# Kernel optimization log

Measured on AMD Instinct MI355X. Metric: run time of the kernel, lower is better.

## Reference

```python
import jax, jax.numpy as jnp
import numpy as np

N = 50000          # nodes
E_RAND = 800000    # random edges (avg degree 16)
D_IN = 128
H = 4              # heads (both layers)
C = 64             # per-head channels (both layers)
NEG_SLOPE = 0.2    # PyG GATConv default leaky_relu slope


def _gat_conv(x, src, dst, W, att_src, att_dst, bias, concat):
    """PyG GATConv (dropout=0, self-loops already in edge list).
    x:[N,Din] W:[Din,H*C] att_*:[H,C] bias:[H*C] or [C]."""
    n = x.shape[0]
    h = (x @ W).reshape(n, H, C)                      # [N,H,C]
    a_src = jnp.sum(h * att_src, axis=-1)             # [N,H]
    a_dst = jnp.sum(h * att_dst, axis=-1)             # [N,H]
    e = jax.nn.leaky_relu(a_src[src] + a_dst[dst], NEG_SLOPE)  # [E,H]
    # segment softmax over incoming edges of each destination node
    m = jax.ops.segment_max(e, dst, num_segments=n)    # [N,H]
    e = jnp.exp(e - m[dst])
    denom = jax.ops.segment_sum(e, dst, num_segments=n)
    alpha = e / (denom[dst] + 1e-16)                   # [E,H]
    msg = h[src] * alpha[..., None]                    # [E,H,C]
    out = jax.ops.segment_sum(msg, dst, num_segments=n)  # [N,H,C]
    if concat:
        out = out.reshape(n, H * C)
    else:
        out = out.mean(axis=1)
    return out + bias


def setup_inputs() -> dict:
    key = jax.random.key(0)
    ks = jax.random.split(key, 10)
    x = jax.random.normal(ks[0], (N, D_IN), jnp.float32)
    src = jax.random.randint(ks[1], (E_RAND,), 0, N)
    dst = jax.random.randint(ks[2], (E_RAND,), 0, N)
    loops = jnp.arange(N)  # add_self_loops=True (PyG default)
    edge_index = jnp.stack([jnp.concatenate([src, loops]),
                            jnp.concatenate([dst, loops])]).astype(jnp.int32)
    g = lambda k, shp, fan: (jax.random.normal(k, shp, jnp.float32) / np.float32(np.sqrt(fan)))
    W1 = g(ks[3], (D_IN, H * C), D_IN)
    att_src1 = g(ks[4], (H, C), C)
    att_dst1 = g(ks[5], (H, C), C)
    b1 = jnp.zeros((H * C,), jnp.float32)
    W2 = g(ks[6], (H * C, H * C), H * C)
    att_src2 = g(ks[7], (H, C), C)
    att_dst2 = g(ks[8], (H, C), C)
    b2 = jnp.zeros((C,), jnp.float32)
    return {"x": x, "edge_index": edge_index,
            "W1": W1, "att_src1": att_src1, "att_dst1": att_dst1, "b1": b1,
            "W2": W2, "att_src2": att_src2, "att_dst2": att_dst2, "b2": b2}


def reference(x, edge_index, W1, att_src1, att_dst1, b1, W2, att_src2, att_dst2, b2):
    src, dst = edge_index[0], edge_index[1]
    h = jax.nn.relu(_gat_conv(x, src, dst, W1, att_src1, att_dst1, b1, concat=True))
    h = jax.nn.relu(_gat_conv(h, src, dst, W2, att_src2, att_dst2, b2, concat=False))
    return jax.nn.softmax(h, axis=1)
```

## Files before the change

### kernel.cpp

```cpp
#include <hip/hip_runtime.h>


typedef __attribute__((ext_vector_type(8))) short short8;
typedef __attribute__((ext_vector_type(4))) float f32x4;
typedef __attribute__((ext_vector_type(2))) float f32x2;

static __device__ __forceinline__ ushort f2bf(float f) {
  uint u = __float_as_uint(f);
  return (ushort)((u + 0x7FFFu + ((u >> 16) & 1u)) >> 16);
}
static __device__ __forceinline__ float bf2f(ushort s) {
  return __uint_as_float(((uint)s) << 16);
}
static __device__ __forceinline__ unsigned char f2fp8(float f) {
  int p = __builtin_amdgcn_cvt_pk_fp8_f32(f, f, 0, false);
  return (unsigned char)(p & 0xFF);
}
static __device__ __forceinline__ uint4 cvt8bf(const float4& a, const float4& b) {
  uint4 hh;
  hh.x = (uint)f2bf(a.x) | ((uint)f2bf(a.y) << 16);
  hh.y = (uint)f2bf(a.z) | ((uint)f2bf(a.w) << 16);
  hh.z = (uint)f2bf(b.x) | ((uint)f2bf(b.y) << 16);
  hh.w = (uint)f2bf(b.z) | ((uint)f2bf(b.w) << 16);
  return hh;
}
static __device__ __forceinline__ void gl16(const ushort* g, ushort* l) {
  __builtin_amdgcn_global_load_lds(
      (const __attribute__((address_space(1))) uint*)(g),
      (__attribute__((address_space(3))) uint*)(l), 16, 0, 0);
}

__global__ __launch_bounds__(256)
void k_prep(const float* __restrict__ W1, const float* __restrict__ W2,
            ushort* __restrict__ w1t, ushort* __restrict__ w2t,
            const float* __restrict__ x, ushort* __restrict__ xb,
            int* __restrict__ cnt, int N,
            int ng , int xcb) {
  const int b = blockIdx.x;
  if (b < 128) {
    int gid = b * 256 + threadIdx.x;
    int c = gid & 255, k = gid >> 8;
    w1t[(size_t)c * 128 + k] = f2bf(W1[(size_t)k * 256 + c]);
  } else if (b < 384) {
    int gid = (b - 128) * 256 + threadIdx.x;
    int c = gid & 255, k = gid >> 8;
    w2t[(size_t)c * 256 + k] = f2bf(W2[(size_t)k * 256 + c]);
  } else if (b < 384 + xcb) {
    int i = (b - 384) * 256 + threadIdx.x;
    if (i < ng) {
      const float4* xp = (const float4*)x + (size_t)i * 2;
      float4 a = xp[0], bb = xp[1];
      ((uint4*)xb)[i] = cvt8bf(a, bb);
    }
  } else {
    int i = (b - 384 - xcb) * 1024 + threadIdx.x;
#pragma unroll
    for (int k = 0; k < 4; k++) {
      int j = i + k * 256;
      if (j < N) cnt[j] = 0;
    }
  }
}

template <int K>
static __device__ __forceinline__
void gemm_body(int bid, const ushort* __restrict__ Ah,
               const ushort* __restrict__ Bt,
               unsigned char* __restrict__ hout, int Nrows,
               const float* __restrict__ att_s, const float* __restrict__ att_d,
               float* __restrict__ a_s, float* __restrict__ a_d) {
  __shared__ ushort Asb[2][128][32];
  __shared__ ushort Bhb[2][128][32];

  const int nrb = (Nrows + 127) >> 7;
  const int rb = (bid >> 4) * 8 + (bid & 7);
  const int ch = (bid >> 3) & 1;
  if (rb >= nrb) return;
  const int row0 = rb * 128;
  const int col0 = ch * 128;

  const int t = threadIdx.x;
  const int lane = t & 63;
  const int w = t >> 6;
  const int wr = (w >> 1) * 64;
  const int wc = (w & 1) * 64;
  const int fr = lane & 15;
  const int fq = lane >> 4;

  const int srow = lane >> 2;
  const int skc = (lane & 3) * 8;
  int ar0 = row0 + w * 32 + srow;
  int ar1 = ar0 + 16;
  ar0 = ar0 < Nrows ? ar0 : Nrows - 1;
  ar1 = ar1 < Nrows ? ar1 : Nrows - 1;
  const ushort* agp0 = Ah + (size_t)ar0 * K + skc;
  const ushort* agp1 = Ah + (size_t)ar1 * K + skc;
  const ushort* bhg0 = Bt + (size_t)(col0 + w * 32 + srow) * K + skc;
  const ushort* bhg1 = bhg0 + (size_t)16 * K;

  f32x4 acc[4][4] = {};

  auto stage = [&](int buf, int k0) {
    gl16(agp0 + k0, &Asb[buf][w * 32][0]);
    gl16(agp1 + k0, &Asb[buf][w * 32 + 16][0]);
    gl16(bhg0 + k0, &Bhb[buf][w * 32][0]);
    gl16(bhg1 + k0, &Bhb[buf][w * 32 + 16][0]);
  };

  stage(0, 0);
  const int NK = K / 32;
#pragma unroll
  for (int ks = 0; ks < NK; ks++) {
    const int buf = ks & 1;
    __syncthreads();
    if (ks + 1 < NK) stage(buf ^ 1, (ks + 1) * 32);

    short8 fa[4], fbh[4];
#pragma unroll
    for (int r = 0; r < 4; r++)
      fa[r] = *(const short8*)(&Asb[buf][wr + r * 16 + fr][fq * 8]);
#pragma unroll
    for (int c = 0; c < 4; c++)
      fbh[c] = *(const short8*)(&Bhb[buf][wc + c * 16 + fr][fq * 8]);
#pragma unroll
    for (int r = 0; r < 4; r++)
#pragma unroll
      for (int c = 0; c < 4; c++)
        acc[r][c] = __builtin_amdgcn_mfma_f32_16x16x32_bf16(fa[r], fbh[c], acc[r][c], 0, 0, 0);
  }

#pragma unroll
  for (int r = 0; r < 4; r++)
#pragma unroll
    for (int c = 0; c < 4; c++) {
      int colg = col0 + wc + c * 16 + fr;
#pragma unroll
      for (int reg = 0; reg < 4; reg++) {
        int gr = row0 + wr + r * 16 + fq * 4 + reg;
        if (gr < Nrows)
          hout[(size_t)gr * 256 + colg] = f2fp8(acc[r][c][reg]);
      }
    }

  const int head = (col0 + wc) >> 6;
  float asv[4], adv[4];
#pragma unroll
  for (int c = 0; c < 4; c++) {
    asv[c] = att_s[col0 + wc + c * 16 + fr];
    adv[c] = att_d[col0 + wc + c * 16 + fr];
  }
#pragma unroll
  for (int r = 0; r < 4; r++)
#pragma unroll
    for (int reg = 0; reg < 4; reg++) {
      float ps = 0.f, pd = 0.f;
#pragma unroll
      for (int c = 0; c < 4; c++) {
        ps += acc[r][c][reg] * asv[c];
        pd += acc[r][c][reg] * adv[c];
      }
      ps += __shfl_xor(ps, 1); pd += __shfl_xor(pd, 1);
      ps += __shfl_xor(ps, 2); pd += __shfl_xor(pd, 2);
      ps += __shfl_xor(ps, 4); pd += __shfl_xor(pd, 4);
      ps += __shfl_xor(ps, 8); pd += __shfl_xor(pd, 8);
      if (fr == 0) {
        int gr = row0 + wr + r * 16 + fq * 4 + reg;
        if (gr < Nrows) {
          a_s[(size_t)gr * 4 + head] = ps;
          a_d[(size_t)gr * 4 + head] = pd;
        }
      }
    }
}

__global__ __launch_bounds__(256)
void k_gemm1_hist(const ushort* __restrict__ xb,
                  const ushort* __restrict__ Bt,
                  unsigned char* __restrict__ hout, int Nrows,
                  const float* __restrict__ att_s,
                  const float* __restrict__ att_d,
                  float* __restrict__ a_s, float* __restrict__ a_d,
                  const int* __restrict__ srcv, const int* __restrict__ dstv,
                  int* __restrict__ cnt, int* __restrict__ col2,
                  int E, int gemm_blocks) {
  if ((int)blockIdx.x < gemm_blocks) {
    gemm_body<128>(blockIdx.x, xb, Bt, hout, Nrows,
                   att_s, att_d, a_s, a_d);
  } else {
    int base = ((int)blockIdx.x - gemm_blocks) * 2048 + threadIdx.x;
    int d[8], v[8], s[8];
#pragma unroll
    for (int k = 0; k < 8; k++) {
      int i = base + k * 256;
      bool ok = i < E;
      d[k] = ok ? dstv[i] : 0;
      v[k] = ok ? (srcv[i] << 8) : 0;
    }
#pragma unroll
    for (int k = 0; k < 8; k++) {
      int i = base + k * 256;
      s[k] = (i < E) ? atomicAdd(&cnt[d[k]], 1) : 64;
    }
#pragma unroll
    for (int k = 0; k < 8; k++) {
      int i = base + k * 256;
      if (i < E && s[k] < 64) col2[(d[k] << 6) + s[k]] = v[k];
    }
  }
}

__global__ __launch_bounds__(256)
void k_gemm2(const ushort* __restrict__ Ah,
             const ushort* __restrict__ Bt,
             unsigned char* __restrict__ hout, int Nrows,
             const float* __restrict__ att_s, const float* __restrict__ att_d,
             float* __restrict__ a_s, float* __restrict__ a_d) {
  gemm_body<256>(blockIdx.x, Ah, Bt, hout, Nrows,
                 att_s, att_d, a_s, a_d);
}

template <int LAYER>
__global__ __launch_bounds__(256)
void k_aggr(const unsigned char* __restrict__ hsrc,
            const int* __restrict__ cnt, const int* __restrict__ col2,
            const float* __restrict__ a_s, const float* __restrict__ a_d,
            const float* __restrict__ bias,
            ushort* __restrict__ out_h, float* __restrict__ outp, int N) {
  __shared__ int   s_sh[4][64];
  __shared__ float w_sh[4][256];
  const int wv = threadIdx.x >> 6;
  const int lane = threadIdx.x & 63;
  const int node = blockIdx.x * 4 + wv;
  if (node >= N) return;
  const int hd = lane >> 4;
  const int deg = min(cnt[node], 64);
  const int beg = node << 6;
  const float4 adst = *(const float4*)(a_d + (size_t)node * 4);

  f32x2 accA = {0.f, 0.f};
  f32x2 accB = {0.f, 0.f};
  float wsum = 0.f;
  const char* hbase = (const char*)hsrc + lane * 4;

  {
    int nc = deg;
    int off = 0;
    float4 w4 = make_float4(0.f, 0.f, 0.f, 0.f);
    if (lane < nc) {
      off = col2[beg + lane];
      const float4 a = *(const float4*)((const char*)a_s + (size_t)((uint)off >> 4));
      float e0 = a.x + adst.x; e0 = e0 > 0.f ? e0 : 0.2f * e0;
      float e1 = a.y + adst.y; e1 = e1 > 0.f ? e1 : 0.2f * e1;
      float e2 = a.z + adst.z; e2 = e2 > 0.f ? e2 : 0.2f * e2;
      float e3 = a.w + adst.w; e3 = e3 > 0.f ? e3 : 0.2f * e3;
      w4 = make_float4(__expf(e0), __expf(e1), __expf(e2), __expf(e3));
    }
    s_sh[wv][lane] = off;
    *(float4*)(&w_sh[wv][lane * 4]) = w4;
    asm volatile("s_waitcnt lgkmcnt(0)" ::: "memory");

    const float* wrow = &w_sh[wv][hd];
    const int*   srow = &s_sh[wv][0];
    int j = 0;
    for (; j + 8 <= nc; j += 8) {
      int o0 = srow[j],     o1 = srow[j + 1], o2 = srow[j + 2], o3 = srow[j + 3];
      int o4 = srow[j + 4], o5 = srow[j + 5], o6 = srow[j + 6], o7 = srow[j + 7];
      float ww0 = wrow[4 * j],      ww1 = wrow[4 * j + 4];
      float ww2 = wrow[4 * j + 8],  ww3 = wrow[4 * j + 12];
      float ww4 = wrow[4 * j + 16], ww5 = wrow[4 * j + 20];
      float ww6 = wrow[4 * j + 24], ww7 = wrow[4 * j + 28];
      uint p0 = *(const uint*)(hbase + (size_t)(uint)o0);
      uint p1 = *(const uint*)(hbase + (size_t)(uint)o1);
      uint p2 = *(const uint*)(hbase + (size_t)(uint)o2);
      uint p3 = *(const uint*)(hbase + (size_t)(uint)o3);
      uint p4 = *(const uint*)(hbase + (size_t)(uint)o4);
      uint p5 = *(const uint*)(hbase + (size_t)(uint)o5);
      uint p6 = *(const uint*)(hbase + (size_t)(uint)o6);
      uint p7 = *(const uint*)(hbase + (size_t)(uint)o7);
      wsum += ww0 + ww1 + ww2 + ww3;
      wsum += ww4 + ww5 + ww6 + ww7;
      f32x2 W;
#define EDGE_FMA(ww, p)                                                     \
      {                                                                     \
        f32x2 lo = __builtin_amdgcn_cvt_pk_f32_fp8((p), false);             \
        f32x2 hi = __builtin_amdgcn_cvt_pk_f32_fp8((p), true);              \
        W.x = (ww); W.y = (ww);                                             \
        accA = __builtin_elementwise_fma(W, lo, accA);                      \
        accB = __builtin_elementwise_fma(W, hi, accB);                      \
      }
      EDGE_FMA(ww0, p0) EDGE_FMA(ww1, p1) EDGE_FMA(ww2, p2) EDGE_FMA(ww3, p3)
      EDGE_FMA(ww4, p4) EDGE_FMA(ww5, p5) EDGE_FMA(ww6, p6) EDGE_FMA(ww7, p7)
    }
    for (; j + 4 <= nc; j += 4) {
      int o0 = srow[j], o1 = srow[j + 1], o2 = srow[j + 2], o3 = srow[j + 3];
      float ww0 = wrow[4 * j],     ww1 = wrow[4 * j + 4];
      float ww2 = wrow[4 * j + 8], ww3 = wrow[4 * j + 12];
      uint p0 = *(const uint*)(hbase + (size_t)(uint)o0);
      uint p1 = *(const uint*)(hbase + (size_t)(uint)o1);
      uint p2 = *(const uint*)(hbase + (size_t)(uint)o2);
      uint p3 = *(const uint*)(hbase + (size_t)(uint)o3);
      wsum += ww0 + ww1 + ww2 + ww3;
      f32x2 W;
      EDGE_FMA(ww0, p0) EDGE_FMA(ww1, p1) EDGE_FMA(ww2, p2) EDGE_FMA(ww3, p3)
    }
    for (; j < nc; j++) {
      int o = srow[j];
      float ww = wrow[4 * j];
      uint p = *(const uint*)(hbase + (size_t)(uint)o);
      wsum += ww;
      f32x2 W;
      EDGE_FMA(ww, p)
    }
#undef EDGE_FMA
  }

  float inv = 1.0f / wsum;
  float4 v = make_float4(accA.x * inv, accA.y * inv, accB.x * inv, accB.y * inv);

  if (LAYER == 1) {
    const float4 bv = *(const float4*)(bias + lane * 4);
    v.x = fmaxf(v.x + bv.x, 0.f);
    v.y = fmaxf(v.y + bv.y, 0.f);
    v.z = fmaxf(v.z + bv.z, 0.f);
    v.w = fmaxf(v.w + bv.w, 0.f);
    ushort4 h;
    h.x = f2bf(v.x); h.y = f2bf(v.y); h.z = f2bf(v.z); h.w = f2bf(v.w);
    *(ushort4*)(out_h + (size_t)node * 256 + lane * 4) = h;
  } else {
    v.x += __shfl_xor(v.x, 16); v.y += __shfl_xor(v.y, 16);
    v.z += __shfl_xor(v.z, 16); v.w += __shfl_xor(v.w, 16);
    v.x += __shfl_xor(v.x, 32); v.y += __shfl_xor(v.y, 32);
    v.z += __shfl_xor(v.z, 32); v.w += __shfl_xor(v.w, 32);
    const int c4 = (lane & 15) * 4;
    const float4 bv = *(const float4*)(bias + c4);
    v.x = fmaxf(v.x * 0.25f + bv.x, 0.f);
    v.y = fmaxf(v.y * 0.25f + bv.y, 0.f);
    v.z = fmaxf(v.z * 0.25f + bv.z, 0.f);
    v.w = fmaxf(v.w * 0.25f + bv.w, 0.f);
    float mx = fmaxf(fmaxf(v.x, v.y), fmaxf(v.z, v.w));
    for (int off = 8; off >= 1; off >>= 1) mx = fmaxf(mx, __shfl_xor(mx, off));
    v.x = __expf(v.x - mx); v.y = __expf(v.y - mx);
    v.z = __expf(v.z - mx); v.w = __expf(v.w - mx);
    float sum = v.x + v.y + v.z + v.w;
    for (int off = 8; off >= 1; off >>= 1) sum += __shfl_xor(sum, off);
    float is = 1.0f / sum;
    v.x *= is; v.y *= is; v.z *= is; v.w *= is;
    if (lane < 16) *(float4*)(outp + (size_t)node * 64 + c4) = v;
  }
}


extern "C" void kernel_launch(void* const* d_in, const int* in_sizes, int n_in,
                              void* d_out, int out_size, void* d_ws, size_t ws_size,
                              hipStream_t stream) {
  const float* x   = (const float*)d_in[0];
  const int*   ei  = (const int*)d_in[1];
  const float* W1  = (const float*)d_in[2];
  const float* as1 = (const float*)d_in[3];
  const float* ad1 = (const float*)d_in[4];
  const float* b1  = (const float*)d_in[5];
  const float* W2  = (const float*)d_in[6];
  const float* as2 = (const float*)d_in[7];
  const float* ad2 = (const float*)d_in[8];
  const float* b2  = (const float*)d_in[9];
  float* out = (float*)d_out;

  const int N = in_sizes[0] / 128;
  const int E = in_sizes[1] / 2;
  const int* srcv = ei;
  const int* dstv = ei + E;

  unsigned char* h8 = (unsigned char*)d_ws;
  ushort* hb   = (ushort*)(h8 + (size_t)N * 256);
  ushort* w1t  = hb + (size_t)N * 256;
  ushort* w2t  = w1t + 256 * 128;
  float*  zbuf = (float*)(w2t + 256 * 256);
  float* a_s1 = zbuf;
  float* a_d1 = a_s1 + (size_t)N * 4;
  float* a_s2 = a_d1 + (size_t)N * 4;
  float* a_d2 = a_s2 + (size_t)N * 4;
  int* cnt    = (int*)(zbuf + (size_t)N * 16);
  int* col2   = cnt + N;
  ushort* xb  = (ushort*)(col2 + (size_t)N * 64);

  const int eb8 = (E + 2047) / 2048;
  const int ng = N * 16;
  const int xcb = (ng + 255) / 256;
  const int zb  = (N + 1023) / 1024;

  const int nrb = (N + 127) / 128;
  const int gemm_blocks = ((nrb + 7) / 8) * 16;
  const int wb = (N + 3) / 4;

  k_prep<<<384 + xcb + zb, 256, 0, stream>>>(W1, W2, w1t, w2t,
                                             x, xb, cnt, N, ng, xcb);
  k_gemm1_hist<<<gemm_blocks + eb8, 256, 0, stream>>>(
      xb, w1t, h8, N, as1, ad1, a_s1, a_d1,
      srcv, dstv, cnt, col2, E, gemm_blocks);
  k_aggr<1><<<wb, 256, 0, stream>>>(h8, cnt, col2, a_s1, a_d1, b1,
                                    hb, nullptr, N);
  k_gemm2<<<gemm_blocks, 256, 0, stream>>>(hb, w2t, h8, N,
                                           as2, ad2, a_s2, a_d2);
  k_aggr<2><<<wb, 256, 0, stream>>>(h8, cnt, col2, a_s2, a_d2, b2,
                                    nullptr, out, N);
}
```

Baseline: 249.7 us.

## Move edge histogram into prep kernel and zero counts with memset

```diff
diff --git a/kernel.cpp b/kernel.cpp
--- a/kernel.cpp
+++ b/kernel.cpp
@@ -31,33 +31,47 @@
 }
 
 __global__ __launch_bounds__(256)
-void k_prep(const float* __restrict__ W1, const float* __restrict__ W2,
-            ushort* __restrict__ w1t, ushort* __restrict__ w2t,
-            const float* __restrict__ x, ushort* __restrict__ xb,
-            int* __restrict__ cnt, int N,
-            int ng , int xcb) {
+void k_prep_hist(const float* __restrict__ W1, const float* __restrict__ W2,
+                 ushort* __restrict__ w1t, ushort* __restrict__ w2t,
+                 const float* __restrict__ x, ushort* __restrict__ xb,
+                 const int* __restrict__ srcv, const int* __restrict__ dstv,
+                 int* __restrict__ cnt, int* __restrict__ col2,
+                 int E, int ng, int eb8) {
   const int b = blockIdx.x;
-  if (b < 128) {
-    int gid = b * 256 + threadIdx.x;
+  if (b < eb8) {
+    int base = b * 2048 + threadIdx.x;
+    int d[8], v[8], s[8];
+#pragma unroll
+    for (int k = 0; k < 8; k++) {
+      int i = base + k * 256;
+      bool ok = i < E;
+      d[k] = ok ? dstv[i] : 0;
+      v[k] = ok ? (srcv[i] << 8) : 0;
+    }
+#pragma unroll
+    for (int k = 0; k < 8; k++) {
+      int i = base + k * 256;
+      s[k] = (i < E) ? atomicAdd(&cnt[d[k]], 1) : 64;
+    }
+#pragma unroll
+    for (int k = 0; k < 8; k++) {
+      int i = base + k * 256;
+      if (i < E && s[k] < 64) col2[(d[k] << 6) + s[k]] = v[k];
+    }
+  } else if (b < eb8 + 128) {
+    int gid = (b - eb8) * 256 + threadIdx.x;
     int c = gid & 255, k = gid >> 8;
     w1t[(size_t)c * 128 + k] = f2bf(W1[(size_t)k * 256 + c]);
-  } else if (b < 384) {
-    int gid = (b - 128) * 256 + threadIdx.x;
+  } else if (b < eb8 + 384) {
+    int gid = (b - eb8 - 128) * 256 + threadIdx.x;
     int c = gid & 255, k = gid >> 8;
     w2t[(size_t)c * 256 + k] = f2bf(W2[(size_t)k * 256 + c]);
-  } else if (b < 384 + xcb) {
-    int i = (b - 384) * 256 + threadIdx.x;
+  } else {
+    int i = (b - eb8 - 384) * 256 + threadIdx.x;
     if (i < ng) {
       const float4* xp = (const float4*)x + (size_t)i * 2;
       float4 a = xp[0], bb = xp[1];
       ((uint4*)xb)[i] = cvt8bf(a, bb);
-    }
-  } else {
-    int i = (b - 384 - xcb) * 1024 + threadIdx.x;
-#pragma unroll
-    for (int k = 0; k < 4; k++) {
-      int j = i + k * 256;
-      if (j < N) cnt[j] = 0;
     }
   }
 }
@@ -174,49 +188,19 @@
 }
 
 __global__ __launch_bounds__(256)
-void k_gemm1_hist(const ushort* __restrict__ xb,
-                  const ushort* __restrict__ Bt,
-                  unsigned char* __restrict__ hout, int Nrows,
-                  const float* __restrict__ att_s,
-                  const float* __restrict__ att_d,
-                  float* __restrict__ a_s, float* __restrict__ a_d,
-                  const int* __restrict__ srcv, const int* __restrict__ dstv,
-                  int* __restrict__ cnt, int* __restrict__ col2,
-                  int E, int gemm_blocks) {
-  if ((int)blockIdx.x < gemm_blocks) {
-    gemm_body<128>(blockIdx.x, xb, Bt, hout, Nrows,
-                   att_s, att_d, a_s, a_d);
-  } else {
-    int base = ((int)blockIdx.x - gemm_blocks) * 2048 + threadIdx.x;
-    int d[8], v[8], s[8];
-#pragma unroll
-    for (int k = 0; k < 8; k++) {
-      int i = base + k * 256;
-      bool ok = i < E;
-      d[k] = ok ? dstv[i] : 0;
-      v[k] = ok ? (srcv[i] << 8) : 0;
-    }
-#pragma unroll
-    for (int k = 0; k < 8; k++) {
-      int i = base + k * 256;
-      s[k] = (i < E) ? atomicAdd(&cnt[d[k]], 1) : 64;
-    }
-#pragma unroll
-    for (int k = 0; k < 8; k++) {
-      int i = base + k * 256;
-      if (i < E && s[k] < 64) col2[(d[k] << 6) + s[k]] = v[k];
-    }
-  }
-}
-
-__global__ __launch_bounds__(256)
-void k_gemm2(const ushort* __restrict__ Ah,
-             const ushort* __restrict__ Bt,
+void k_gemm1(const ushort* __restrict__ xb, const ushort* __restrict__ Bt,
              unsigned char* __restrict__ hout, int Nrows,
              const float* __restrict__ att_s, const float* __restrict__ att_d,
              float* __restrict__ a_s, float* __restrict__ a_d) {
-  gemm_body<256>(blockIdx.x, Ah, Bt, hout, Nrows,
-                 att_s, att_d, a_s, a_d);
+  gemm_body<128>(blockIdx.x, xb, Bt, hout, Nrows, att_s, att_d, a_s, a_d);
+}
+
+__global__ __launch_bounds__(256)
+void k_gemm2(const ushort* __restrict__ Ah, const ushort* __restrict__ Bt,
+             unsigned char* __restrict__ hout, int Nrows,
+             const float* __restrict__ att_s, const float* __restrict__ att_d,
+             float* __restrict__ a_s, float* __restrict__ a_d) {
+  gemm_body<256>(blockIdx.x, Ah, Bt, hout, Nrows, att_s, att_d, a_s, a_d);
 }
 
 template <int LAYER>
@@ -386,17 +370,16 @@
   const int eb8 = (E + 2047) / 2048;
   const int ng = N * 16;
   const int xcb = (ng + 255) / 256;
-  const int zb  = (N + 1023) / 1024;
 
   const int nrb = (N + 127) / 128;
   const int gemm_blocks = ((nrb + 7) / 8) * 16;
   const int wb = (N + 3) / 4;
 
-  k_prep<<<384 + xcb + zb, 256, 0, stream>>>(W1, W2, w1t, w2t,
-                                             x, xb, cnt, N, ng, xcb);
-  k_gemm1_hist<<<gemm_blocks + eb8, 256, 0, stream>>>(
-      xb, w1t, h8, N, as1, ad1, a_s1, a_d1,
-      srcv, dstv, cnt, col2, E, gemm_blocks);
+  hipMemsetAsync(cnt, 0, (size_t)N * 4, stream);
+  k_prep_hist<<<eb8 + 384 + xcb, 256, 0, stream>>>(
+      W1, W2, w1t, w2t, x, xb, srcv, dstv, cnt, col2, E, ng, eb8);
+  k_gemm1<<<gemm_blocks, 256, 0, stream>>>(xb, w1t, h8, N,
+                                           as1, ad1, a_s1, a_d1);
   k_aggr<1><<<wb, 256, 0, stream>>>(h8, cnt, col2, a_s1, a_d1, b1,
                                     hb, nullptr, N);
   k_gemm2<<<gemm_blocks, 256, 0, stream>>>(hb, w2t, h8, N,
```

New measurement: 269.7 us. +8.0%, slower.
